# Kernel optimization log

Hardware: AMD Instinct MI355X
Metric: run time of the kernel (lower is better)

Reference implementation:

```python
import jax, jax.numpy as jnp
import numpy as np

B, N, D = 256, 200000, 64
ACT_DIM, N_WP, N_ACT, H = 6, 512, 32, 64
SAME_WP_MIN = 8

def setup_inputs() -> dict:
    key = jax.random.key(0)
    ks = jax.random.split(key, 12)
    return {
        'q': jax.random.normal(ks[0], (B, D), jnp.float32),
        'library_vecs': jax.random.normal(ks[1], (N, D), jnp.float32),
        'retrieval_mask': jax.random.uniform(ks[2], (B, N)) < 0.1,
        'library_waypoint_ids': jax.random.randint(ks[3], (N,), 0, N_WP),
        'waypoint_id': jax.random.randint(ks[4], (B,), 0, N_WP),
        'action_id': jax.random.randint(ks[5], (B,), 0, N_ACT),
        'wp_action_prior': jax.random.uniform(ks[6], (B,), jnp.float32),
        'action_emb': jax.random.normal(ks[7], (N_ACT, ACT_DIM), jnp.float32) * 0.1,
        'W1': jax.random.normal(ks[8], (2 * D + ACT_DIM, H), jnp.float32) * (1.0 / np.sqrt(2 * D + ACT_DIM)),
        'b1': jnp.zeros((H,), jnp.float32),
        'W2': jax.random.normal(ks[9], (H, 1), jnp.float32) * (1.0 / np.sqrt(H)),
        'b2': jnp.zeros((1,), jnp.float32),
        'log_tau': jnp.asarray(np.log(0.5), jnp.float32),
        'prior_logit_weight': jnp.asarray(1.5, jnp.float32),
    }

def reference(q, library_vecs, retrieval_mask, library_waypoint_ids,
              waypoint_id, action_id, wp_action_prior, action_emb,
              W1, b1, W2, b2, log_tau, prior_logit_weight):
    NEG_INF = jnp.float32(-jnp.inf)
    tau = jnp.clip(jnp.exp(log_tau), 1e-3, 10.0)
    # [B, N] scores
    scores = jnp.einsum('bd,nd->bn', q, library_vecs) / tau
    scores = jnp.where(retrieval_mask, NEG_INF, scores)
    # same-waypoint hard filter
    wp_match = library_waypoint_ids[None, :] == waypoint_id[:, None]  # [B, N]
    valid_same_wp = wp_match & ~retrieval_mask
    same_wp_count = valid_same_wp.sum(axis=-1)
    sufficient = same_wp_count >= SAME_WP_MIN  # [B]
    wp_filter = (~wp_match) & sufficient[:, None]
    scores = jnp.where(wp_filter, NEG_INF, scores)
    attn = jax.nn.softmax(scores, axis=-1)  # [B, N]
    context = jnp.einsum('bn,nd->bd', attn, library_vecs)  # [B, D]
    action_vec = action_emb[action_id]  # [B, ACT_DIM]
    h = jnp.concatenate([q, context, action_vec], axis=-1)  # [B, 2D+ACT_DIM]
    h1 = jax.nn.gelu(h @ W1 + b1, approximate=False)
    logits = (h1 @ W2 + b2)[:, 0]  # [B]
    prior = jnp.clip(wp_action_prior, 1e-3, 1.0 - 1e-3)
    prior_logit = jnp.log(prior) - jnp.log1p(-prior)
    logits = logits + prior_logit_weight * prior_logit
    return logits, attn
```

## Files before the change

### kernel.cpp

```cpp
#include <hip/hip_runtime.h>
#include <cmath>

#define Nn 200000
#define CAP 1024
#define CAPQ 256
#define ESZ 25000
#define EI4 6250
#define NIT 98
#define NF4 50000

__device__ __forceinline__ bool mask_at(const void* m, size_t idx, int isbyte) {
    if (isbyte) return ((const unsigned char*)m)[idx] != 0;
    return ((const unsigned int*)m)[idx] != 0u;
}

__global__ __launch_bounds__(512) void kmain(
    const float* __restrict__ q, const float* __restrict__ lib,
    const void* __restrict__ mask, const int* __restrict__ lib_wp,
    const int* __restrict__ wp_id, const int* __restrict__ action_id,
    const float* __restrict__ wp_prior, const float* __restrict__ act_emb,
    const float* __restrict__ W1, const float* __restrict__ b1,
    const float* __restrict__ W2, const float* __restrict__ b2,
    const float* __restrict__ log_tau, const float* __restrict__ plw,
    float* __restrict__ out) {
    __shared__ int qlist[8 * CAPQ];
    __shared__ int qcnt[8];
    __shared__ int nlist[CAP];
    __shared__ float svals[CAP];
    __shared__ unsigned char vbit[CAP];
    __shared__ float ltile[64 * 65];
    __shared__ float q_s[64], pbuf[64], ctx_s[64];
    __shared__ float redm[8], reds[8];
    __shared__ float pbuf2[512];
    __shared__ int redci[512];
    __shared__ float MshD, SshD, Mf, iSf;
    __shared__ int isb_s, dense_s, sz_s;

    int b = blockIdx.x, t = threadIdx.x;
    int wv = t >> 6, lane = t & 63;
    float* attnrow = out + 256 + (size_t)b * Nn;
    int wpb = wp_id[b];

    if (wv == 0) {
        const uint4* mw4 = (const uint4*)mask;
        int f = 0;
        for (int i = lane; i < 1024; i += 64) {
            uint4 x = mw4[i];
            if ((x.x >= 2u && x.x != 0x3F800000u) || (x.y >= 2u && x.y != 0x3F800000u) ||
                (x.z >= 2u && x.z != 0x3F800000u) || (x.w >= 2u && x.w != 0x3F800000u))
                f = 1;
        }
        unsigned long long bal = __ballot(f != 0);
        if (lane == 0) isb_s = bal ? 1 : 0;
    }
    {
        const int4* seg = (const int4*)(lib_wp + wv * ESZ);
        int cnt = 0;
        int pad = wpb ^ 1;
#pragma unroll 4
        for (int it = 0; it < NIT; ++it) {
            int i = it * 64 + lane;
            int4 v = (i < EI4) ? seg[i] : make_int4(pad, pad, pad, pad);
            int m0 = (v.x == wpb) ? 1 : 0;
            int m1 = (v.y == wpb) ? 1 : 0;
            int m2 = (v.z == wpb) ? 1 : 0;
            int m3 = (v.w == wpb) ? 1 : 0;
            int mc = m0 + m1 + m2 + m3;
            unsigned long long anyb = __ballot(mc != 0);
            if (anyb) {
                int inc = mc;
#pragma unroll
                for (int o = 1; o < 64; o <<= 1) {
                    int x = __shfl_up(inc, o, 64);
                    if (lane >= o) inc += x;
                }
                int excl = inc - mc;
                int wtot = __shfl(inc, 63, 64);
                int pos = cnt + excl;
                int nb = wv * ESZ + i * 4;
                if (m0) { if (pos < CAPQ) qlist[wv * CAPQ + pos] = nb;     pos++; }
                if (m1) { if (pos < CAPQ) qlist[wv * CAPQ + pos] = nb + 1; pos++; }
                if (m2) { if (pos < CAPQ) qlist[wv * CAPQ + pos] = nb + 2; pos++; }
                if (m3) { if (pos < CAPQ) qlist[wv * CAPQ + pos] = nb + 3; pos++; }
                cnt += wtot;
            }
        }
        if (lane == 0) qcnt[wv] = cnt;
    }
    __syncthreads();

    if (wv == 0) {
        int isb = isb_s;
        int cs[8];
        int sz = 0;
        bool ov = false;
#pragma unroll
        for (int k = 0; k < 8; ++k) {
            int c = qcnt[k];
            cs[k] = c; sz += c;
            if (c > CAPQ) ov = true;
        }
        if (sz > CAP) ov = true;
        int cntv = 0;
        if (!ov) {
            int base = 0;
#pragma unroll
            for (int k = 0; k < 8; ++k) {
                for (int i = lane; i < cs[k]; i += 64) nlist[base + i] = qlist[k * CAPQ + i];
                base += cs[k];
            }
            asm volatile("s_waitcnt lgkmcnt(0)" ::: "memory");
            for (int i = lane; i < sz; i += 64) {
                int n = nlist[i];
                bool v = !mask_at(mask, (size_t)b * Nn + n, isb);
                vbit[i] = v ? 1 : 0;
                cntv += v ? 1 : 0;
            }
#pragma unroll
            for (int o = 1; o < 64; o <<= 1) cntv += __shfl_xor(cntv, o, 64);
        }
        bool sf = (!ov) && (cntv >= 8);
        if (lane == 0) { dense_s = sf ? 0 : 1; sz_s = sz; }
        if (sf) {
            q_s[lane] = q[b * 64 + lane];
            float tau = expf(log_tau[0]);
            tau = fminf(fmaxf(tau, 1e-3f), 10.0f);
            float inv_tau = 1.0f / tau;
            float Ms = -INFINITY, Ss = 0.f, ctxp = 0.f;
            for (int cc = 0; cc < sz; cc += 64) {
                int cn = min(64, sz - cc);
                if (lane < cn) {
                    int n_i = nlist[cc + lane];
                    const float4* src = (const float4*)&lib[(size_t)n_i * 64];
                    float* dst = &ltile[lane * 65];
#pragma unroll
                    for (int p4 = 0; p4 < 16; ++p4) {
                        float4 v = src[p4];
                        dst[p4 * 4] = v.x; dst[p4 * 4 + 1] = v.y;
                        dst[p4 * 4 + 2] = v.z; dst[p4 * 4 + 3] = v.w;
                    }
                }
                asm volatile("s_waitcnt lgkmcnt(0)" ::: "memory");
                float s = -INFINITY;
                if (lane < cn && vbit[cc + lane]) {
                    float acc = 0.f;
#pragma unroll
                    for (int dd = 0; dd < 64; ++dd)
                        acc = fmaf(q_s[dd], ltile[lane * 65 + dd], acc);
                    s = acc * inv_tau;
                }
                if (lane < cn) svals[cc + lane] = s;
                float m = s;
#pragma unroll
                for (int o = 1; o < 64; o <<= 1) m = fmaxf(m, __shfl_xor(m, o, 64));
                float e = (s > -INFINITY) ? expf(s - m) : 0.f;
#pragma unroll
                for (int o = 1; o < 64; o <<= 1) e += __shfl_xor(e, o, 64);
                float scl = 1.f;
                float newM = fmaxf(Ms, m);
                if (newM > -INFINITY) {
                    scl = expf(Ms - newM);
                    Ss = Ss * scl + e * expf(m - newM);
                    Ms = newM;
                }
                ctxp *= scl;
                pbuf[lane] = (s > -INFINITY) ? expf(s - Ms) : 0.f;
                asm volatile("s_waitcnt lgkmcnt(0)" ::: "memory");
                for (int i2 = 0; i2 < cn; ++i2)
                    ctxp = fmaf(pbuf[i2], ltile[i2 * 65 + lane], ctxp);
            }
            float invS = 1.0f / Ss;
            ctx_s[lane] = ctxp * invS;
            if (lane == 0) { Mf = Ms; iSf = invS; }
        }
    } else {
        float4* rowp = (float4*)attnrow;
        const float4 z = make_float4(0.f, 0.f, 0.f, 0.f);
        const int share = 7143;
        int s0 = (wv - 1) * share;
        int e0 = min(NF4, s0 + share);
#pragma unroll 4
        for (int i = s0 + lane; i < e0; i += 64) rowp[i] = z;
    }
    __syncthreads();

    int dense = dense_s;
    if (!dense) {
        float M = Mf, invS = iSf;
        int sz = sz_s;
        for (int i = t; i < sz; i += 512) {
            float s2 = svals[i];
            attnrow[nlist[i]] = (s2 > -INFINITY) ? expf(s2 - M) * invS : 0.f;
        }
    } else {
        int isb = isb_s;
        int cntd = 0;
        for (int c0 = 0; c0 < Nn; c0 += 512) {
            int n = c0 + t;
            if (n < Nn && lib_wp[n] == wpb && !mask_at(mask, (size_t)b * Nn + n, isb))
                cntd++;
        }
        redci[t] = cntd;
        __syncthreads();
        for (int s2 = 256; s2 > 0; s2 >>= 1) {
            if (t < s2) redci[t] += redci[t + s2];
            __syncthreads();
        }
        int sfb = (redci[0] >= 8) ? 1 : 0;
        if (t < 64) q_s[t] = q[b * 64 + t];
        if (t == 0) { MshD = -INFINITY; SshD = 0.f; }
        float tau = expf(log_tau[0]);
        tau = fminf(fmaxf(tau, 1e-3f), 10.0f);
        float inv_tau = 1.0f / tau;
        __syncthreads();
        for (int c0 = 0; c0 < Nn; c0 += 512) {
            int n = c0 + t;
            float s = -INFINITY;
            if (n < Nn) {
                bool mk = mask_at(mask, (size_t)b * Nn + n, isb);
                bool wpm = (lib_wp[n] == wpb);
                if (!mk && !(sfb && !wpm)) {
                    float acc = 0.f;
#pragma unroll
                    for (int dd = 0; dd < 64; dd += 4) {
                        float4 v = *(const float4*)&lib[(size_t)n * 64 + dd];
                        acc = fmaf(q_s[dd], v.x, acc);
                        acc = fmaf(q_s[dd + 1], v.y, acc);
                        acc = fmaf(q_s[dd + 2], v.z, acc);
                        acc = fmaf(q_s[dd + 3], v.w, acc);
                    }
                    s = acc * inv_tau;
                }
                attnrow[n] = s;
            }
            float m = s;
#pragma unroll
            for (int o = 1; o < 64; o <<= 1) m = fmaxf(m, __shfl_xor(m, o, 64));
            float e = (s > -INFINITY) ? expf(s - m) : 0.f;
#pragma unroll
            for (int o = 1; o < 64; o <<= 1) e += __shfl_xor(e, o, 64);
            if (lane == 0) { redm[wv] = m; reds[wv] = e; }
            __syncthreads();
            if (t == 0) {
                for (int g = 0; g < 8; ++g) {
                    float m2 = redm[g], e2 = reds[g];
                    if (m2 > -INFINITY) {
                        if (m2 > MshD) { SshD = SshD * expf(MshD - m2) + e2; MshD = m2; }
                        else           { SshD += e2 * expf(m2 - MshD); }
                    }
                }
            }
            __syncthreads();
        }
        float M = MshD, invS = 1.0f / SshD;
        int d = t & 63, g = t >> 6;
        float ctxp = 0.f;
        for (int c0 = 0; c0 < Nn; c0 += 512) {
            int n = c0 + t;
            float p = 0.f;
            if (n < Nn) {
                float s = attnrow[n];
                p = (s > -INFINITY) ? expf(s - M) * invS : 0.f;
                attnrow[n] = p;
            }
            pbuf2[t] = p;
            __syncthreads();
            int lim = min(512, Nn - c0);
            for (int i2 = g; i2 < lim; i2 += 8) {
                float p2 = pbuf2[i2];
                if (p2 != 0.f) ctxp = fmaf(p2, lib[(size_t)(c0 + i2) * 64 + d], ctxp);
            }
            __syncthreads();
        }
        pbuf2[t] = ctxp;
        __syncthreads();
        if (t < 64) {
            float cacc = 0.f;
            for (int g2 = 0; g2 < 8; ++g2) cacc += pbuf2[g2 * 64 + t];
            ctx_s[t] = cacc;
        }
        __syncthreads();
    }

    if (t < 64) {
        int j = t;
        float ctx = ctx_s[j];
        float acc = b1[j];
        int aid = action_id[b];
        for (int i = 0; i < 64; ++i) acc = fmaf(q[b * 64 + i], W1[i * 64 + j], acc);
        for (int i = 0; i < 64; ++i) acc = fmaf(__shfl(ctx, i, 64), W1[(64 + i) * 64 + j], acc);
        for (int i = 0; i < 6; ++i) acc = fmaf(act_emb[aid * 6 + i], W1[(128 + i) * 64 + j], acc);
        float h1 = 0.5f * acc * (1.0f + erff(acc * 0.70710678118654752f));
        float v = h1 * W2[j];
#pragma unroll
        for (int o = 1; o < 64; o <<= 1) v += __shfl_xor(v, o, 64);
        if (j == 0) {
            float pr = fminf(fmaxf(wp_prior[b], 1e-3f), 1.0f - 1e-3f);
            float pl = logf(pr) - log1pf(-pr);
            out[b] = v + b2[0] + plw[0] * pl;
        }
    }
}

extern "C" void kernel_launch(void* const* d_in, const int* in_sizes, int n_in,
                              void* d_out, int out_size, void* d_ws, size_t ws_size,
                              hipStream_t stream) {
    const float* q = (const float*)d_in[0];
    const float* lib = (const float*)d_in[1];
    const void* mask = d_in[2];
    const int* lib_wp = (const int*)d_in[3];
    const int* wp_id = (const int*)d_in[4];
    const int* action_id = (const int*)d_in[5];
    const float* wp_prior = (const float*)d_in[6];
    const float* act_emb = (const float*)d_in[7];
    const float* W1 = (const float*)d_in[8];
    const float* b1 = (const float*)d_in[9];
    const float* W2 = (const float*)d_in[10];
    const float* b2 = (const float*)d_in[11];
    const float* log_tau = (const float*)d_in[12];
    const float* plw = (const float*)d_in[13];
    float* out = (float*)d_out;
    (void)d_ws; (void)ws_size; (void)in_sizes; (void)n_in; (void)out_size;

    kmain<<<dim3(256), 512, 0, stream>>>(q, lib, mask, lib_wp, wp_id, action_id, wp_prior,
                                         act_emb, W1, b1, W2, b2, log_tau, plw, out);
}
```

Baseline: 94.51 us.

## Split into two kernels with grid-wide zero-fill blocks and workspace handoff

Splits the single fused kernel into two launches. The first runs 256 compute blocks that build the sparse candidate list and softmax, writing results to workspace. Alongside them, 768 extra blocks zero the whole output buffer, so the 205 MB attention write is spread over many more CUs than the old 7 waves per block. The second kernel scatters the sparse probabilities, handles the dense fallback and runs the MLP head. This adds a second launch and some workspace traffic, and the zero-fill overwrites the logits region, which k2 later rewrites.

```diff
diff --git a/kernel.cpp b/kernel.cpp
--- a/kernel.cpp
+++ b/kernel.cpp
@@ -7,38 +7,43 @@
 #define ESZ 25000
 #define EI4 6250
 #define NIT 98
-#define NF4 50000
+#define N4TOT 12800064
+#define NCOMP 256
+#define NFILL 768
+#define NBLK1 1024
 
 __device__ __forceinline__ bool mask_at(const void* m, size_t idx, int isbyte) {
     if (isbyte) return ((const unsigned char*)m)[idx] != 0;
     return ((const unsigned int*)m)[idx] != 0u;
 }
 
-__global__ __launch_bounds__(512) void kmain(
+__global__ __launch_bounds__(512) void k1(
     const float* __restrict__ q, const float* __restrict__ lib,
     const void* __restrict__ mask, const int* __restrict__ lib_wp,
-    const int* __restrict__ wp_id, const int* __restrict__ action_id,
-    const float* __restrict__ wp_prior, const float* __restrict__ act_emb,
-    const float* __restrict__ W1, const float* __restrict__ b1,
-    const float* __restrict__ W2, const float* __restrict__ b2,
-    const float* __restrict__ log_tau, const float* __restrict__ plw,
-    float* __restrict__ out) {
+    const int* __restrict__ wp_id, const float* __restrict__ log_tau,
+    float* __restrict__ out,
+    int* __restrict__ nlist_g, float* __restrict__ pv_g, float* __restrict__ ctxws,
+    int* __restrict__ dense_g, int* __restrict__ szr_g, int* __restrict__ isb_g) {
+    int bid = blockIdx.x, t = threadIdx.x;
+    if (bid >= NCOMP) {
+        float4* p = (float4*)out;
+        const float4 z = make_float4(0.f, 0.f, 0.f, 0.f);
+        int stride = NFILL * 512;
+#pragma unroll 4
+        for (int i = (bid - NCOMP) * 512 + t; i < N4TOT; i += stride) p[i] = z;
+        return;
+    }
     __shared__ int qlist[8 * CAPQ];
     __shared__ int qcnt[8];
     __shared__ int nlist[CAP];
     __shared__ float svals[CAP];
     __shared__ unsigned char vbit[CAP];
     __shared__ float ltile[64 * 65];
-    __shared__ float q_s[64], pbuf[64], ctx_s[64];
-    __shared__ float redm[8], reds[8];
-    __shared__ float pbuf2[512];
-    __shared__ int redci[512];
-    __shared__ float MshD, SshD, Mf, iSf;
-    __shared__ int isb_s, dense_s, sz_s;
-
-    int b = blockIdx.x, t = threadIdx.x;
+    __shared__ float q_s[64], pbuf[64];
+    __shared__ int isb_s;
+
+    int b = bid;
     int wv = t >> 6, lane = t & 63;
-    float* attnrow = out + 256 + (size_t)b * Nn;
     int wpb = wp_id[b];
 
     if (wv == 0) {
@@ -88,132 +93,152 @@
         if (lane == 0) qcnt[wv] = cnt;
     }
     __syncthreads();
-
-    if (wv == 0) {
-        int isb = isb_s;
-        int cs[8];
-        int sz = 0;
-        bool ov = false;
+    if (wv != 0) return;
+
+    int isb = isb_s;
+    int cs[8];
+    int sz = 0;
+    bool ov = false;
+#pragma unroll
+    for (int k = 0; k < 8; ++k) {
+        int c = qcnt[k];
+        cs[k] = c; sz += c;
+        if (c > CAPQ) ov = true;
+    }
+    if (sz > CAP) ov = true;
+    int cntv = 0;
+    if (!ov) {
+        int base = 0;
 #pragma unroll
         for (int k = 0; k < 8; ++k) {
-            int c = qcnt[k];
-            cs[k] = c; sz += c;
-            if (c > CAPQ) ov = true;
-        }
-        if (sz > CAP) ov = true;
-        int cntv = 0;
-        if (!ov) {
-            int base = 0;
-#pragma unroll
-            for (int k = 0; k < 8; ++k) {
-                for (int i = lane; i < cs[k]; i += 64) nlist[base + i] = qlist[k * CAPQ + i];
-                base += cs[k];
-            }
-            asm volatile("s_waitcnt lgkmcnt(0)" ::: "memory");
-            for (int i = lane; i < sz; i += 64) {
-                int n = nlist[i];
-                bool v = !mask_at(mask, (size_t)b * Nn + n, isb);
-                vbit[i] = v ? 1 : 0;
-                cntv += v ? 1 : 0;
-            }
-#pragma unroll
-            for (int o = 1; o < 64; o <<= 1) cntv += __shfl_xor(cntv, o, 64);
-        }
-        bool sf = (!ov) && (cntv >= 8);
-        if (lane == 0) { dense_s = sf ? 0 : 1; sz_s = sz; }
-        if (sf) {
-            q_s[lane] = q[b * 64 + lane];
-            float tau = expf(log_tau[0]);
-            tau = fminf(fmaxf(tau, 1e-3f), 10.0f);
-            float inv_tau = 1.0f / tau;
-            float Ms = -INFINITY, Ss = 0.f, ctxp = 0.f;
-            for (int cc = 0; cc < sz; cc += 64) {
-                int cn = min(64, sz - cc);
-                if (lane < cn) {
-                    int n_i = nlist[cc + lane];
-                    const float4* src = (const float4*)&lib[(size_t)n_i * 64];
-                    float* dst = &ltile[lane * 65];
-#pragma unroll
-                    for (int p4 = 0; p4 < 16; ++p4) {
-                        float4 v = src[p4];
-                        dst[p4 * 4] = v.x; dst[p4 * 4 + 1] = v.y;
-                        dst[p4 * 4 + 2] = v.z; dst[p4 * 4 + 3] = v.w;
-                    }
-                }
-                asm volatile("s_waitcnt lgkmcnt(0)" ::: "memory");
-                float s = -INFINITY;
-                if (lane < cn && vbit[cc + lane]) {
-                    float acc = 0.f;
-#pragma unroll
-                    for (int dd = 0; dd < 64; ++dd)
-                        acc = fmaf(q_s[dd], ltile[lane * 65 + dd], acc);
-                    s = acc * inv_tau;
-                }
-                if (lane < cn) svals[cc + lane] = s;
-                float m = s;
-#pragma unroll
-                for (int o = 1; o < 64; o <<= 1) m = fmaxf(m, __shfl_xor(m, o, 64));
-                float e = (s > -INFINITY) ? expf(s - m) : 0.f;
-#pragma unroll
-                for (int o = 1; o < 64; o <<= 1) e += __shfl_xor(e, o, 64);
-                float scl = 1.f;
-                float newM = fmaxf(Ms, m);
-                if (newM > -INFINITY) {
-                    scl = expf(Ms - newM);
-                    Ss = Ss * scl + e * expf(m - newM);
-                    Ms = newM;
-                }
-                ctxp *= scl;
-                pbuf[lane] = (s > -INFINITY) ? expf(s - Ms) : 0.f;
-                asm volatile("s_waitcnt lgkmcnt(0)" ::: "memory");
-                for (int i2 = 0; i2 < cn; ++i2)
-                    ctxp = fmaf(pbuf[i2], ltile[i2 * 65 + lane], ctxp);
-            }
-            float invS = 1.0f / Ss;
-            ctx_s[lane] = ctxp * invS;
-            if (lane == 0) { Mf = Ms; iSf = invS; }
-        }
+            for (int i = lane; i < cs[k]; i += 64) {
+                int n = qlist[k * CAPQ + i];
+                nlist[base + i] = n;
+                nlist_g[(size_t)b * CAP + base + i] = n;
+            }
+            base += cs[k];
+        }
+        asm volatile("s_waitcnt lgkmcnt(0)" ::: "memory");
+        for (int i = lane; i < sz; i += 64) {
+            int n = nlist[i];
+            bool v = !mask_at(mask, (size_t)b * Nn + n, isb);
+            vbit[i] = v ? 1 : 0;
+            cntv += v ? 1 : 0;
+        }
+#pragma unroll
+        for (int o = 1; o < 64; o <<= 1) cntv += __shfl_xor(cntv, o, 64);
+    }
+    bool sf = (!ov) && (cntv >= 8);
+    if (lane == 0) {
+        dense_g[b] = sf ? 0 : 1;
+        szr_g[b] = sz;
+        if (b == 0) isb_g[0] = isb;
+    }
+    if (!sf) return;
+
+    q_s[lane] = q[b * 64 + lane];
+    float tau = expf(log_tau[0]);
+    tau = fminf(fmaxf(tau, 1e-3f), 10.0f);
+    float inv_tau = 1.0f / tau;
+    float Ms = -INFINITY, Ss = 0.f, ctxp = 0.f;
+    for (int cc = 0; cc < sz; cc += 64) {
+        int cn = min(64, sz - cc);
+        if (lane < cn) {
+            int n_i = nlist[cc + lane];
+            const float4* src = (const float4*)&lib[(size_t)n_i * 64];
+            float* dst = &ltile[lane * 65];
+#pragma unroll
+            for (int p4 = 0; p4 < 16; ++p4) {
+                float4 v = src[p4];
+                dst[p4 * 4] = v.x; dst[p4 * 4 + 1] = v.y;
+                dst[p4 * 4 + 2] = v.z; dst[p4 * 4 + 3] = v.w;
+            }
+        }
+        asm volatile("s_waitcnt lgkmcnt(0)" ::: "memory");
+        float s = -INFINITY;
+        if (lane < cn && vbit[cc + lane]) {
+            float acc = 0.f;
+#pragma unroll
+            for (int dd = 0; dd < 64; ++dd)
+                acc = fmaf(q_s[dd], ltile[lane * 65 + dd], acc);
+            s = acc * inv_tau;
+        }
+        if (lane < cn) svals[cc + lane] = s;
+        float m = s;
+#pragma unroll
+        for (int o = 1; o < 64; o <<= 1) m = fmaxf(m, __shfl_xor(m, o, 64));
+        float e = (s > -INFINITY) ? expf(s - m) : 0.f;
+#pragma unroll
+        for (int o = 1; o < 64; o <<= 1) e += __shfl_xor(e, o, 64);
+        float scl = 1.f;
+        float newM = fmaxf(Ms, m);
+        if (newM > -INFINITY) {
+            scl = expf(Ms - newM);
+            Ss = Ss * scl + e * expf(m - newM);
+            Ms = newM;
+        }
+        ctxp *= scl;
+        pbuf[lane] = (s > -INFINITY) ? expf(s - Ms) : 0.f;
+        asm volatile("s_waitcnt lgkmcnt(0)" ::: "memory");
+        for (int i2 = 0; i2 < cn; ++i2)
+            ctxp = fmaf(pbuf[i2], ltile[i2 * 65 + lane], ctxp);
+    }
+    float invS = 1.0f / Ss;
+    ctxws[b * 64 + lane] = ctxp * invS;
+    for (int i = lane; i < sz; i += 64) {
+        float s2 = svals[i];
+        pv_g[(size_t)b * CAP + i] = (s2 > -INFINITY) ? expf(s2 - Ms) * invS : 0.f;
+    }
+}
+
+__global__ __launch_bounds__(256) void k2(
+    const float* __restrict__ q, const float* __restrict__ lib,
+    const void* __restrict__ mask, const int* __restrict__ lib_wp,
+    const int* __restrict__ wp_id, const int* __restrict__ action_id,
+    const float* __restrict__ wp_prior, const float* __restrict__ act_emb,
+    const float* __restrict__ W1, const float* __restrict__ b1,
+    const float* __restrict__ W2, const float* __restrict__ b2,
+    const float* __restrict__ log_tau, const float* __restrict__ plw,
+    float* __restrict__ out,
+    const int* __restrict__ nlist_g, const float* __restrict__ pv_g,
+    float* __restrict__ ctxws, const int* __restrict__ dense_g,
+    const int* __restrict__ szr_g, const int* __restrict__ isb_g) {
+    __shared__ float q_s[64];
+    __shared__ float redm[4], reds[4];
+    __shared__ float Msh, Ssh;
+    __shared__ float pbuf2[256];
+    __shared__ int redci[256];
+    int b = blockIdx.x, t = threadIdx.x;
+    float* attnrow = out + 256 + (size_t)b * Nn;
+    int dense = dense_g[b];
+    int wpb = wp_id[b];
+
+    if (!dense) {
+        int sz = szr_g[b];
+        for (int i = t; i < sz; i += 256)
+            attnrow[nlist_g[(size_t)b * CAP + i]] = pv_g[(size_t)b * CAP + i];
     } else {
-        float4* rowp = (float4*)attnrow;
-        const float4 z = make_float4(0.f, 0.f, 0.f, 0.f);
-        const int share = 7143;
-        int s0 = (wv - 1) * share;
-        int e0 = min(NF4, s0 + share);
-#pragma unroll 4
-        for (int i = s0 + lane; i < e0; i += 64) rowp[i] = z;
-    }
-    __syncthreads();
-
-    int dense = dense_s;
-    if (!dense) {
-        float M = Mf, invS = iSf;
-        int sz = sz_s;
-        for (int i = t; i < sz; i += 512) {
-            float s2 = svals[i];
-            attnrow[nlist[i]] = (s2 > -INFINITY) ? expf(s2 - M) * invS : 0.f;
-        }
-    } else {
-        int isb = isb_s;
+        int isb = isb_g[0];
         int cntd = 0;
-        for (int c0 = 0; c0 < Nn; c0 += 512) {
+        for (int c0 = 0; c0 < Nn; c0 += 256) {
             int n = c0 + t;
             if (n < Nn && lib_wp[n] == wpb && !mask_at(mask, (size_t)b * Nn + n, isb))
                 cntd++;
         }
         redci[t] = cntd;
         __syncthreads();
-        for (int s2 = 256; s2 > 0; s2 >>= 1) {
+        for (int s2 = 128; s2 > 0; s2 >>= 1) {
             if (t < s2) redci[t] += redci[t + s2];
             __syncthreads();
         }
         int sfb = (redci[0] >= 8) ? 1 : 0;
         if (t < 64) q_s[t] = q[b * 64 + t];
-        if (t == 0) { MshD = -INFINITY; SshD = 0.f; }
+        if (t == 0) { Msh = -INFINITY; Ssh = 0.f; }
         float tau = expf(log_tau[0]);
         tau = fminf(fmaxf(tau, 1e-3f), 10.0f);
         float inv_tau = 1.0f / tau;
         __syncthreads();
-        for (int c0 = 0; c0 < Nn; c0 += 512) {
+        for (int c0 = 0; c0 < Nn; c0 += 256) {
             int n = c0 + t;
             float s = -INFINITY;
             if (n < Nn) {
@@ -239,23 +264,23 @@
             float e = (s > -INFINITY) ? expf(s - m) : 0.f;
 #pragma unroll
             for (int o = 1; o < 64; o <<= 1) e += __shfl_xor(e, o, 64);
-            if (lane == 0) { redm[wv] = m; reds[wv] = e; }
+            if ((t & 63) == 0) { redm[t >> 6] = m; reds[t >> 6] = e; }
             __syncthreads();
             if (t == 0) {
-                for (int g = 0; g < 8; ++g) {
+                for (int g = 0; g < 4; ++g) {
                     float m2 = redm[g], e2 = reds[g];
                     if (m2 > -INFINITY) {
-                        if (m2 > MshD) { SshD = SshD * expf(MshD - m2) + e2; MshD = m2; }
-                        else           { SshD += e2 * expf(m2 - MshD); }
+                        if (m2 > Msh) { Ssh = Ssh * expf(Msh - m2) + e2; Msh = m2; }
+                        else          { Ssh += e2 * expf(m2 - Msh); }
                     }
                 }
             }
             __syncthreads();
         }
-        float M = MshD, invS = 1.0f / SshD;
+        float M = Msh, invS = 1.0f / Ssh;
         int d = t & 63, g = t >> 6;
         float ctxp = 0.f;
-        for (int c0 = 0; c0 < Nn; c0 += 512) {
+        for (int c0 = 0; c0 < Nn; c0 += 256) {
             int n = c0 + t;
             float p = 0.f;
             if (n < Nn) {
@@ -265,8 +290,8 @@
             }
             pbuf2[t] = p;
             __syncthreads();
-            int lim = min(512, Nn - c0);
-            for (int i2 = g; i2 < lim; i2 += 8) {
+            int lim = min(256, Nn - c0);
+            for (int i2 = g; i2 < lim; i2 += 4) {
                 float p2 = pbuf2[i2];
                 if (p2 != 0.f) ctxp = fmaf(p2, lib[(size_t)(c0 + i2) * 64 + d], ctxp);
             }
@@ -274,17 +299,13 @@
         }
         pbuf2[t] = ctxp;
         __syncthreads();
-        if (t < 64) {
-            float cacc = 0.f;
-            for (int g2 = 0; g2 < 8; ++g2) cacc += pbuf2[g2 * 64 + t];
-            ctx_s[t] = cacc;
-        }
-        __syncthreads();
-    }
-
+        if (t < 64)
+            ctxws[b * 64 + t] = pbuf2[t] + pbuf2[64 + t] + pbuf2[128 + t] + pbuf2[192 + t];
+    }
+    __syncthreads();
     if (t < 64) {
         int j = t;
-        float ctx = ctx_s[j];
+        float ctx = ctxws[b * 64 + j];
         float acc = b1[j];
         int aid = action_id[b];
         for (int i = 0; i < 64; ++i) acc = fmaf(q[b * 64 + i], W1[i * 64 + j], acc);
@@ -320,8 +341,18 @@
     const float* log_tau = (const float*)d_in[12];
     const float* plw = (const float*)d_in[13];
     float* out = (float*)d_out;
-    (void)d_ws; (void)ws_size; (void)in_sizes; (void)n_in; (void)out_size;
-
-    kmain<<<dim3(256), 512, 0, stream>>>(q, lib, mask, lib_wp, wp_id, action_id, wp_prior,
-                                         act_emb, W1, b1, W2, b2, log_tau, plw, out);
+
+    char* ws = (char*)d_ws;
+    int* dense_g = (int*)(ws + 0);
+    int* szr_g   = (int*)(ws + 1024);
+    int* isb_g   = (int*)(ws + 2048);
+    float* ctxws = (float*)(ws + 4096);
+    int* nlist_g = (int*)(ws + 69632);
+    float* pv_g  = (float*)(ws + 69632 + 1048576);
+
+    k1<<<dim3(NBLK1), 512, 0, stream>>>(q, lib, mask, lib_wp, wp_id, log_tau, out,
+                                        nlist_g, pv_g, ctxws, dense_g, szr_g, isb_g);
+    k2<<<dim3(256), 256, 0, stream>>>(q, lib, mask, lib_wp, wp_id, action_id, wp_prior,
+                                      act_emb, W1, b1, W2, b2, log_tau, plw, out,
+                                      nlist_g, pv_g, ctxws, dense_g, szr_g, isb_g);
 }
```

Result: slower. 97.26 us (+2.9%).
